# Kernel optimization log

Hardware: AMD Instinct MI355X
Metric: run time of the kernel (lower is better)

The kernel has to match this reference:

```python
import jax, jax.numpy as jnp
import numpy as np
import itertools

DIM_X, DIM_Y = 3, 3
MAX_DIGIT = DIM_X * DIM_Y          # 9
NUM_NODES = MAX_DIGIT ** 2         # 81
EMBED = 16
HID = 96
BATCH = 256
ITERS = 4


def determine_edges(dim_x, dim_y):
    md = dim_x * dim_y
    rows = []
    for r in range(md):
        for c in range(md):
            s = {(r, i) for i in range(md)} | {(i, c) for i in range(md)}
            xm, ym = r // dim_x * dim_x, c // dim_y * dim_y
            s |= set(itertools.product(range(xm, xm + dim_x), range(ym, ym + dim_y)))
            s -= {(r, c)}
            rows.append(sorted(i * md + j for i, j in s))
    return np.asarray(rows, dtype=np.int32)  # [81, 20]


def mlp3(x, w0, b0, w1, b1, w2, b2):
    # MLP([a,b,c,d]): two ReLU hidden layers, linear output
    x = jax.nn.relu(x @ w0.T + b0)
    x = jax.nn.relu(x @ w1.T + b1)
    return x @ w2.T + b2


def setup_inputs() -> dict:
    key = jax.random.key(0)
    keys = iter(jax.random.split(key, 40))

    def lin(din, dout):
        kw, kb = jax.random.split(next(keys))
        lim = 1.0 / np.sqrt(din)
        w = jax.random.uniform(kw, (dout, din), jnp.float32, -lim, lim)
        b = jax.random.uniform(kb, (dout,), jnp.float32, -lim, lim)
        return w, b

    embed = jax.random.normal(next(keys), (MAX_DIGIT + 1, EMBED), jnp.float32)

    in_w0, in_b0 = lin(EMBED, HID); in_w1, in_b1 = lin(HID, HID); in_w2, in_b2 = lin(HID, HID)
    f_w0, f_b0 = lin(2 * HID, HID); f_w1, f_b1 = lin(HID, HID); f_w2, f_b2 = lin(HID, HID)
    g_w0, g_b0 = lin(2 * HID, HID); g_w1, g_b1 = lin(HID, HID); g_w2, g_b2 = lin(HID, HID)
    r_w0, r_b0 = lin(HID, HID); r_w1, r_b1 = lin(HID, HID); r_w2, r_b2 = lin(HID, MAX_DIGIT)

    lim = 1.0 / np.sqrt(HID)
    lstm_wih = jax.random.uniform(next(keys), (4 * HID, HID), jnp.float32, -lim, lim)
    lstm_whh = jax.random.uniform(next(keys), (4 * HID, HID), jnp.float32, -lim, lim)
    lstm_bih = jax.random.uniform(next(keys), (4 * HID,), jnp.float32, -lim, lim)
    lstm_bhh = jax.random.uniform(next(keys), (4 * HID,), jnp.float32, -lim, lim)

    grids = jax.random.randint(next(keys), (BATCH, NUM_NODES), 0, MAX_DIGIT + 1)
    c0 = jax.random.normal(next(keys), (BATCH * NUM_NODES, HID), jnp.float32)
    edges = jnp.asarray(determine_edges(DIM_X, DIM_Y))

    return dict(embed=embed,
                in_w0=in_w0, in_b0=in_b0, in_w1=in_w1, in_b1=in_b1, in_w2=in_w2, in_b2=in_b2,
                f_w0=f_w0, f_b0=f_b0, f_w1=f_w1, f_b1=f_b1, f_w2=f_w2, f_b2=f_b2,
                g_w0=g_w0, g_b0=g_b0, g_w1=g_w1, g_b1=g_b1, g_w2=g_w2, g_b2=g_b2,
                lstm_wih=lstm_wih, lstm_whh=lstm_whh, lstm_bih=lstm_bih, lstm_bhh=lstm_bhh,
                r_w0=r_w0, r_b0=r_b0, r_w1=r_w1, r_b1=r_b1, r_w2=r_w2, r_b2=r_b2,
                c0=c0, grids=grids, edges=edges, iters=ITERS)


def reference(embed,
              in_w0, in_b0, in_w1, in_b1, in_w2, in_b2,
              f_w0, f_b0, f_w1, f_b1, f_w2, f_b2,
              g_w0, g_b0, g_w1, g_b1, g_w2, g_b2,
              lstm_wih, lstm_whh, lstm_bih, lstm_bhh,
              r_w0, r_b0, r_w1, r_b1, r_w2, r_b2,
              c0, grids, edges, iters):
    B, N = grids.shape
    K = edges.shape[1]
    emb = embed[grids]                                   # [B, N, EMBED]
    X = mlp3(emb, in_w0, in_b0, in_w1, in_b1, in_w2, in_b2)  # [B, N, HID]
    H = X
    h = X.reshape(B * N, HID)
    c = c0
    outputs = []
    for _ in range(iters):
        # gather neighbor states: [B, N, K, HID]
        Hn = H[:, edges]
        Hs = jnp.broadcast_to(H[:, :, None, :], Hn.shape)
        pair = jnp.concatenate([Hs, Hn], axis=-1)        # [B, N, K, 2*HID]
        M = mlp3(pair, f_w0, f_b0, f_w1, f_b1, f_w2, f_b2).sum(axis=2)  # [B, N, HID]
        gin = mlp3(jnp.concatenate([X, M], axis=-1),
                   g_w0, g_b0, g_w1, g_b1, g_w2, g_b2).reshape(B * N, HID)
        # single-step LSTM (torch gate order: i, f, g, o)
        gates = gin @ lstm_wih.T + lstm_bih + h @ lstm_whh.T + lstm_bhh
        gi, gf, gg, go = jnp.split(gates, 4, axis=-1)
        c = jax.nn.sigmoid(gf) * c + jax.nn.sigmoid(gi) * jnp.tanh(gg)
        h = jax.nn.sigmoid(go) * jnp.tanh(c)
        H = h.reshape(B, N, HID)
        outputs.append(mlp3(H, r_w0, r_b0, r_w1, r_b1, r_w2, r_b2))  # [B, N, MAX_DIGIT]
    return jnp.stack(outputs)  # [iters, B, N, MAX_DIGIT]
```

## Files before the change

### kernel.cpp

```cpp
#include <hip/hip_runtime.h>
#include <hip/hip_bf16.h>

typedef __hip_bfloat16 bf16;
typedef __attribute__((ext_vector_type(8))) short short8;
typedef __attribute__((ext_vector_type(8))) __bf16 bf16x8;
typedef __attribute__((ext_vector_type(4))) float f32x4;

#define BN 20736
#define NNODE 81
#define KNB 20

__device__ inline float bf2f(short s) {
  union { unsigned u; float f; } x; x.u = ((unsigned)(unsigned short)s) << 16; return x.f;
}
__device__ inline short f2bf(float f) {
  __hip_bfloat16 h = __float2bfloat16(f);
  return *reinterpret_cast<short*>(&h);
}
__device__ inline bf16x8 ld8(const bf16* p) {
  return __builtin_bit_cast(bf16x8, *(const short8*)p);
}

__device__ inline void zacc3(f32x4 acc[3]) {
  #pragma unroll
  for (int nt = 0; nt < 3; ++nt) acc[nt] = (f32x4){0.f, 0.f, 0.f, 0.f};
}
__device__ inline void load_w48(const bf16* __restrict__ W, int ldw, int n0, int lr, int lq,
                                bf16x8 wf[3][3]) {
  #pragma unroll
  for (int nt = 0; nt < 3; ++nt)
    #pragma unroll
    for (int ks = 0; ks < 3; ++ks)
      wf[nt][ks] = ld8(&W[(size_t)(n0 + nt * 16 + lr) * ldw + ks * 32 + lq * 8]);
}
__device__ inline void gemm48(const bf16x8 af[3], const bf16x8 wf[3][3], f32x4 acc[3]) {
  #pragma unroll
  for (int ks = 0; ks < 3; ++ks)
    #pragma unroll
    for (int nt = 0; nt < 3; ++nt)
      acc[nt] = __builtin_amdgcn_mfma_f32_16x16x32_bf16(af[ks], wf[nt][ks], acc[nt], 0, 0, 0);
}
__device__ inline void acc_store_cs(float* xw, const f32x4 acc[3], int lr, int lq, int n0) {
  #pragma unroll
  for (int nt = 0; nt < 3; ++nt)
    #pragma unroll
    for (int r = 0; r < 4; ++r)
      xw[(lq * 4 + r) * 100 + n0 + nt * 16 + lr] = acc[nt][r];
}
__device__ inline void xbuf_frag(const float* xw, int lr, int lq,
                                 const float* __restrict__ bias, float bscale,
                                 const bf16* residRow, int act,
                                 bf16x8 af[3]) {
  #pragma unroll
  for (int ks = 0; ks < 3; ++ks) {
    const int c0 = ks * 32 + lq * 8;
    float4 x0 = *(const float4*)&xw[lr * 100 + c0];
    float4 x1 = *(const float4*)&xw[lr * 100 + c0 + 4];
    float xv[8] = {x0.x, x0.y, x0.z, x0.w, x1.x, x1.y, x1.z, x1.w};
    if (bias) {
      float4 b0 = *(const float4*)&bias[c0];
      float4 b1 = *(const float4*)&bias[c0 + 4];
      float bv[8] = {b0.x, b0.y, b0.z, b0.w, b1.x, b1.y, b1.z, b1.w};
      #pragma unroll
      for (int j = 0; j < 8; ++j) xv[j] += bscale * bv[j];
    }
    if (residRow) {
      short8 r8 = *(const short8*)&residRow[c0];
      #pragma unroll
      for (int j = 0; j < 8; ++j) xv[j] += bf2f(r8[j]);
    }
    short8 o;
    #pragma unroll
    for (int j = 0; j < 8; ++j) {
      float v = xv[j];
      if (act) v = fmaxf(v, 0.f);
      o[j] = f2bf(v);
    }
    af[ks] = __builtin_bit_cast(bf16x8, o);
  }
}
__device__ inline void store_frag(bf16* dst, int lq, const bf16x8 af[3]) {
  #pragma unroll
  for (int ks = 0; ks < 3; ++ks)
    *(short8*)&dst[ks * 32 + lq * 8] = __builtin_bit_cast(short8, af[ks]);
}

__global__ __launch_bounds__(256) void prep_k(
    const float* in_w1, const float* in_w2, const float* f_w1, const float* f_w2,
    const float* g_w1, const float* g_w2, const float* r_w0, const float* r_w1,
    const float* r_w2, const float* wih, const float* whh, const float* g_w0,
    const float* f_w0, const float* in_w0, const float* f_b0,
    bf16* inw1b, bf16* inw2b, bf16* fw1b, bf16* fw2b,
    bf16* gw1b, bf16* gw2b, bf16* rw0b, bf16* rw1b,
    bf16* rw2b, bf16* wihb, bf16* whhb, bf16* gw0b,
    bf16* wfnb, bf16* w0pb, float* bias_fn)
{
  int idx = blockIdx.x * 256 + threadIdx.x;
  int y = blockIdx.y;
  const float* src = nullptr; bf16* dst = nullptr; int cnt = 0;
  switch (y) {
    case 0:  src = in_w1; dst = inw1b; cnt = 9216;  break;
    case 1:  src = in_w2; dst = inw2b; cnt = 9216;  break;
    case 2:  src = f_w1;  dst = fw1b;  cnt = 9216;  break;
    case 3:  src = f_w2;  dst = fw2b;  cnt = 9216;  break;
    case 4:  src = g_w1;  dst = gw1b;  cnt = 9216;  break;
    case 5:  src = g_w2;  dst = gw2b;  cnt = 9216;  break;
    case 6:  src = r_w0;  dst = rw0b;  cnt = 9216;  break;
    case 7:  src = r_w1;  dst = rw1b;  cnt = 9216;  break;
    case 8:  src = r_w2;  dst = rw2b;  cnt = 864;   break;
    case 9:  src = wih;   dst = wihb;  cnt = 36864; break;
    case 10: src = whh;   dst = whhb;  cnt = 36864; break;
    case 11: src = g_w0;  dst = gw0b;  cnt = 18432; break;
    case 12: {
      if (idx < 18432) {
        int n = idx / 96, k = idx - n * 96;
        float v = (n < 96) ? f_w0[n * 192 + k] : f_w0[(n - 96) * 192 + 96 + k];
        wfnb[idx] = __float2bfloat16(v);
      }
      return;
    }
    case 13: {
      if (idx < 3072) {
        int n = idx >> 5, k = idx & 31;
        w0pb[idx] = __float2bfloat16(k < 16 ? in_w0[n * 16 + k] : 0.f);
      }
      return;
    }
    default: {
      if (idx < 192) bias_fn[idx] = (idx < 96) ? f_b0[idx] : 0.f;
      return;
    }
  }
  if (idx < cnt) dst[idx] = __float2bfloat16(src[idx]);
}

__global__ __launch_bounds__(256) void prep2_k(
    const float* __restrict__ g_w0, const float* __restrict__ f_w2,
    const float* __restrict__ f_b2, const float* __restrict__ wih,
    const float* __restrict__ g_w2, const float* __restrict__ g_b2,
    const float* __restrict__ bih, const float* __restrict__ bhh,
    bf16* __restrict__ wmcb, float* __restrict__ b_mc,
    bf16* __restrict__ wgcb, float* __restrict__ b_lc)
{
  int idx = blockIdx.x * 256 + threadIdx.x;
  if (idx < 9216) {
    int n = idx / 96, k = idx - n * 96;
    float s = 0.f;
    for (int j = 0; j < 96; ++j) s += g_w0[n * 192 + 96 + j] * f_w2[j * 96 + k];
    wmcb[idx] = __float2bfloat16(s);
  } else if (idx < 9216 + 36864) {
    int r = idx - 9216;
    int m = r / 96, k = r - m * 96;
    float s = 0.f;
    for (int j = 0; j < 96; ++j) s += wih[m * 96 + j] * g_w2[j * 96 + k];
    wgcb[r] = __float2bfloat16(s);
  } else if (idx < 9216 + 36864 + 96) {
    int n = idx - 9216 - 36864;
    float s = 0.f;
    for (int j = 0; j < 96; ++j) s += g_w0[n * 192 + 96 + j] * 20.f * f_b2[j];
    b_mc[n] = s;
  } else if (idx < 9216 + 36864 + 96 + 384) {
    int m = idx - 9216 - 36864 - 96;
    float s = bih[m] + bhh[m];
    for (int j = 0; j < 96; ++j) s += wih[m * 96 + j] * g_b2[j];
    b_lc[m] = s;
  }
}

__global__ __launch_bounds__(256) void fused_in_k(
    const float* __restrict__ embed, const int* __restrict__ grids,
    const bf16* __restrict__ w0pb, const float* __restrict__ in_b0,
    const bf16* __restrict__ inw1b, const float* __restrict__ in_b1,
    const bf16* __restrict__ inw2b, const float* __restrict__ in_b2,
    const bf16* __restrict__ gw0b, const float* __restrict__ g_b0,
    const bf16* __restrict__ wfnb, const float* __restrict__ bias_fn,
    bf16* __restrict__ X, bf16* __restrict__ Xg, bf16* __restrict__ P)
{
  __shared__ float xbuf[2][2][1600];
  const int t = threadIdx.x, w = t >> 6, lane = t & 63, lr = lane & 15, lq = lane >> 4;
  const int mh = w >> 1, ch = w & 1, n0 = ch * 48;
  const int m0 = blockIdx.x * 32 + mh * 16;
  float* x0 = xbuf[0][mh];
  float* x1 = xbuf[1][mh];
  bf16x8 wf[3][3]; f32x4 acc[3]; bf16x8 af[3];

  short8 es = {0, 0, 0, 0, 0, 0, 0, 0};
  if (lq < 2) {
    int gidx = grids[m0 + lr];
    float4 e0 = *(const float4*)&embed[gidx * 16 + lq * 8];
    float4 e1 = *(const float4*)&embed[gidx * 16 + lq * 8 + 4];
    es[0] = f2bf(e0.x); es[1] = f2bf(e0.y); es[2] = f2bf(e0.z); es[3] = f2bf(e0.w);
    es[4] = f2bf(e1.x); es[5] = f2bf(e1.y); es[6] = f2bf(e1.z); es[7] = f2bf(e1.w);
  }
  bf16x8 a0 = __builtin_bit_cast(bf16x8, es);
  #pragma unroll
  for (int nt = 0; nt < 3; ++nt)
    wf[nt][0] = ld8(&w0pb[(size_t)(n0 + nt * 16 + lr) * 32 + lq * 8]);
  zacc3(acc);
  #pragma unroll
  for (int nt = 0; nt < 3; ++nt)
    acc[nt] = __builtin_amdgcn_mfma_f32_16x16x32_bf16(a0, wf[nt][0], acc[nt], 0, 0, 0);
  acc_store_cs(x0, acc, lr, lq, n0);
  __syncthreads();
  xbuf_frag(x0, lr, lq, in_b0, 1.f, nullptr, 1, af);
  load_w48(inw1b, 96, n0, lr, lq, wf); zacc3(acc); gemm48(af, wf, acc);
  acc_store_cs(x1, acc, lr, lq, n0);
  __syncthreads();
  xbuf_frag(x1, lr, lq, in_b1, 1.f, nullptr, 1, af);
  load_w48(inw2b, 96, n0, lr, lq, wf); zacc3(acc); gemm48(af, wf, acc);
  acc_store_cs(x0, acc, lr, lq, n0);
  __syncthreads();
  bf16x8 xf[3];
  xbuf_frag(x0, lr, lq, in_b2, 1.f, nullptr, 0, xf);
  if (ch == 0) store_frag(&X[(size_t)(m0 + lr) * 96], lq, xf);
  load_w48(gw0b, 192, n0, lr, lq, wf); zacc3(acc); gemm48(xf, wf, acc);
  acc_store_cs(x1, acc, lr, lq, n0);
  __syncthreads();
  xbuf_frag(x1, lr, lq, g_b0, 1.f, nullptr, 0, af);
  if (ch == 0) store_frag(&Xg[(size_t)(m0 + lr) * 96], lq, af);
  #pragma unroll
  for (int ph = 0; ph < 2; ++ph) {
    float* xb = ph ? x1 : x0;
    load_w48(wfnb + (size_t)ph * 96 * 96, 96, n0, lr, lq, wf); zacc3(acc); gemm48(xf, wf, acc);
    acc_store_cs(xb, acc, lr, lq, n0);
    __syncthreads();
    xbuf_frag(xb, lr, lq, bias_fn + ph * 96, 1.f, nullptr, 0, af);
    if (ch == 0) store_frag(&P[(size_t)(m0 + lr) * 192 + ph * 96], lq, af);
  }
}

__global__ __launch_bounds__(128) void edge_k(
    const bf16* __restrict__ P, const bf16* __restrict__ w1bf,
    const float* __restrict__ b1, const int* __restrict__ edges,
    bf16* __restrict__ S)
{
  __shared__ short zs[80 * 104];
  const int t = threadIdx.x;
  const int grp = (blockIdx.x & 7) * 648 + (blockIdx.x >> 3);
  const int w = t >> 6, lane = t & 63, lr = lane & 15, lq = lane >> 4;
  const int n0 = w * 48;

  bf16x8 wf1[3][3];
  #pragma unroll
  for (int nt = 0; nt < 3; ++nt)
    #pragma unroll
    for (int ks = 0; ks < 3; ++ks)
      wf1[nt][ks] = ld8(&w1bf[(size_t)(n0 + nt * 16 + lr) * 96 + ks * 32 + lq * 8]);
  float b1v[3];
  #pragma unroll
  for (int nt = 0; nt < 3; ++nt) b1v[nt] = b1[n0 + nt * 16 + lr];

  for (int cc = t; cc < 80 * 12; cc += 128) {
    int row = cc / 12, c8 = cc - row * 12;
    int p = row / 20, j = row - p * 20;
    int gr = grp * 4 + p;
    int b = gr / NNODE, i = gr - b * NNODE;
    int e = edges[i * KNB + j];
    short8 a8 = *(const short8*)&P[(size_t)gr * 192 + c8 * 8];
    short8 n8 = *(const short8*)&P[((size_t)b * NNODE + e) * 192 + 96 + c8 * 8];
    short8 z;
    #pragma unroll
    for (int q = 0; q < 8; ++q)
      z[q] = f2bf(fmaxf(bf2f(a8[q]) + bf2f(n8[q]), 0.f));
    *(short8*)&zs[row * 104 + c8 * 8] = z;
  }
  __syncthreads();

  f32x4 acc[5][3];
  #pragma unroll
  for (int mt = 0; mt < 5; ++mt)
    #pragma unroll
    for (int nt = 0; nt < 3; ++nt) acc[mt][nt] = (f32x4){0.f, 0.f, 0.f, 0.f};
  #pragma unroll
  for (int ks = 0; ks < 3; ++ks) {
    const int koff = ks * 32 + lq * 8;
    #pragma unroll
    for (int mt = 0; mt < 5; ++mt) {
      bf16x8 af = __builtin_bit_cast(bf16x8, *(const short8*)&zs[(mt * 16 + lr) * 104 + koff]);
      #pragma unroll
      for (int nt = 0; nt < 3; ++nt)
        acc[mt][nt] = __builtin_amdgcn_mfma_f32_16x16x32_bf16(af, wf1[nt][ks], acc[mt][nt], 0, 0, 0);
    }
  }

  float nodeacc[4][3];
  #pragma unroll
  for (int pp = 0; pp < 4; ++pp)
    #pragma unroll
    for (int nt = 0; nt < 3; ++nt) nodeacc[pp][nt] = 0.f;
  #pragma unroll
  for (int mt = 0; mt < 5; ++mt)
    #pragma unroll
    for (int nt = 0; nt < 3; ++nt)
      #pragma unroll
      for (int r = 0; r < 4; ++r) {
        int row = mt * 16 + lq * 4 + r;
        int p = row / 20;
        float v = fmaxf(acc[mt][nt][r] + b1v[nt], 0.f);
        #pragma unroll
        for (int pp = 0; pp < 4; ++pp)
          nodeacc[pp][nt] += (p == pp) ? v : 0.f;
      }
  #pragma unroll
  for (int pp = 0; pp < 4; ++pp)
    #pragma unroll
    for (int nt = 0; nt < 3; ++nt) {
      float v = nodeacc[pp][nt];
      v += __shfl_xor(v, 16, 64);
      v += __shfl_xor(v, 32, 64);
      if (lq == 0)
        S[(size_t)(grp * 4 + pp) * 96 + n0 + nt * 16 + lr] = __float2bfloat16(v);
    }
}

__global__ __launch_bounds__(128) void fused_iter_k(
    const bf16* __restrict__ Sin,
    const bf16* __restrict__ wmcb, const float* __restrict__ b_mc,
    const bf16* __restrict__ Xg,
    const bf16* __restrict__ gw1b, const float* __restrict__ g_b1,
    const bf16* __restrict__ Hin,
    const bf16* __restrict__ wgcb, const bf16* __restrict__ whhb,
    const float* __restrict__ b_lc,
    float* __restrict__ c, bf16* __restrict__ Hout,
    const bf16* __restrict__ wfnb, const float* __restrict__ bias_fn, bf16* __restrict__ P,
    const bf16* __restrict__ rw0b, const float* __restrict__ r_b0,
    const bf16* __restrict__ rw1b, const float* __restrict__ r_b1,
    const bf16* __restrict__ rw2b, const float* __restrict__ r_b2,
    float* __restrict__ outp, int doP)
{
  __shared__ float xb0[1600], xb1[1600];
  const int t = threadIdx.x, w = t >> 6, lane = t & 63, lr = lane & 15, lq = lane >> 4;
  const int n0 = w * 48;
  const int m0 = blockIdx.x * 16;

  bf16x8 wfA[3][3], wfB[3][3], af[3];
  f32x4 acc[3];

  #pragma unroll
  for (int ks = 0; ks < 3; ++ks)
    af[ks] = ld8(&Sin[(size_t)(m0 + lr) * 96 + ks * 32 + lq * 8]);
  bf16x8 hin[3];
  #pragma unroll
  for (int ks = 0; ks < 3; ++ks)
    hin[ks] = ld8(&Hin[(size_t)(m0 + lr) * 96 + ks * 32 + lq * 8]);

  load_w48(wmcb, 96, n0, lr, lq, wfA);
  zacc3(acc); gemm48(af, wfA, acc);
  load_w48(gw1b, 96, n0, lr, lq, wfB);
  acc_store_cs(xb0, acc, lr, lq, n0);
  __syncthreads();
  xbuf_frag(xb0, lr, lq, b_mc, 1.f, &Xg[(size_t)(m0 + lr) * 96], 1, af);
  zacc3(acc); gemm48(af, wfB, acc);
  acc_store_cs(xb1, acc, lr, lq, n0);
  float cv[3][4];
  #pragma unroll
  for (int nt = 0; nt < 3; ++nt)
    #pragma unroll
    for (int r = 0; r < 4; ++r)
      cv[nt][r] = c[(size_t)(m0 + lq * 4 + r) * 96 + n0 + nt * 16 + lr];
  __syncthreads();
  bf16x8 zf[3];
  xbuf_frag(xb1, lr, lq, g_b1, 1.f, nullptr, 1, zf);

  f32x4 ga[4][3];
  #pragma unroll
  for (int g4 = 0; g4 < 4; ++g4)
    #pragma unroll
    for (int nt = 0; nt < 3; ++nt) ga[g4][nt] = (f32x4){0.f, 0.f, 0.f, 0.f};
  #pragma unroll
  for (int g4 = 0; g4 < 4; ++g4)
    #pragma unroll
    for (int nt = 0; nt < 3; ++nt) {
      size_t nrow = (size_t)(g4 * 96 + n0 + nt * 16 + lr) * 96;
      #pragma unroll
      for (int ks = 0; ks < 3; ++ks) {
        ga[g4][nt] = __builtin_amdgcn_mfma_f32_16x16x32_bf16(
            zf[ks], ld8(&wgcb[nrow + ks * 32 + lq * 8]), ga[g4][nt], 0, 0, 0);
        ga[g4][nt] = __builtin_amdgcn_mfma_f32_16x16x32_bf16(
            hin[ks], ld8(&whhb[nrow + ks * 32 + lq * 8]), ga[g4][nt], 0, 0, 0);
      }
    }
  #pragma unroll
  for (int nt = 0; nt < 3; ++nt) {
    int col = n0 + nt * 16 + lr;
    float bvi = b_lc[col];
    float bvf = b_lc[96 + col];
    float bvg = b_lc[192 + col];
    float bvo = b_lc[288 + col];
    #pragma unroll
    for (int r = 0; r < 4; ++r) {
      int m = m0 + lq * 4 + r;
      size_t idx = (size_t)m * 96 + col;
      float gi = ga[0][nt][r] + bvi;
      float gfv = ga[1][nt][r] + bvf;
      float gg = ga[2][nt][r] + bvg;
      float go = ga[3][nt][r] + bvo;
      float si = 1.f / (1.f + expf(-gi));
      float sf = 1.f / (1.f + expf(-gfv));
      float so = 1.f / (1.f + expf(-go));
      float tg = tanhf(gg);
      float cn = sf * cv[nt][r] + si * tg;
      float ho = so * tanhf(cn);
      if (doP) {
        c[idx] = cn;
        Hout[idx] = __float2bfloat16(ho);
      }
      xb0[(lq * 4 + r) * 100 + col] = ho;
    }
  }
  __syncthreads();
  bf16x8 hf[3];
  xbuf_frag(xb0, lr, lq, nullptr, 0.f, nullptr, 0, hf);

  if (doP) {
    load_w48(wfnb, 96, n0, lr, lq, wfA);
    zacc3(acc); gemm48(hf, wfA, acc);
    load_w48(wfnb + 96 * 96, 96, n0, lr, lq, wfB);
    #pragma unroll
    for (int nt = 0; nt < 3; ++nt) {
      int col = n0 + nt * 16 + lr;
      float bvv = bias_fn[col];
      #pragma unroll
      for (int r = 0; r < 4; ++r)
        P[(size_t)(m0 + lq * 4 + r) * 192 + col] = __float2bfloat16(acc[nt][r] + bvv);
    }
    zacc3(acc); gemm48(hf, wfB, acc);
    #pragma unroll
    for (int nt = 0; nt < 3; ++nt) {
      int col = n0 + nt * 16 + lr;
      float bvv = bias_fn[96 + col];
      #pragma unroll
      for (int r = 0; r < 4; ++r)
        P[(size_t)(m0 + lq * 4 + r) * 192 + 96 + col] = __float2bfloat16(acc[nt][r] + bvv);
    }
  }

  load_w48(rw0b, 96, n0, lr, lq, wfA);
  zacc3(acc); gemm48(hf, wfA, acc);
  load_w48(rw1b, 96, n0, lr, lq, wfB);
  acc_store_cs(xb1, acc, lr, lq, n0);
  __syncthreads();
  xbuf_frag(xb1, lr, lq, r_b0, 1.f, nullptr, 1, af);
  zacc3(acc); gemm48(af, wfB, acc);
  acc_store_cs(xb0, acc, lr, lq, n0);
  __syncthreads();
  xbuf_frag(xb0, lr, lq, r_b1, 1.f, nullptr, 1, af);
  if (w == 0) {
    bf16x8 w9[3];
    #pragma unroll
    for (int ks = 0; ks < 3; ++ks) {
      short8 s = {0, 0, 0, 0, 0, 0, 0, 0};
      if (lr < 9) s = *(const short8*)&rw2b[(size_t)lr * 96 + ks * 32 + lq * 8];
      w9[ks] = __builtin_bit_cast(bf16x8, s);
    }
    f32x4 a9 = (f32x4){0.f, 0.f, 0.f, 0.f};
    #pragma unroll
    for (int ks = 0; ks < 3; ++ks)
      a9 = __builtin_amdgcn_mfma_f32_16x16x32_bf16(af[ks], w9[ks], a9, 0, 0, 0);
    if (lr < 9) {
      float bb = r_b2[lr];
      #pragma unroll
      for (int r = 0; r < 4; ++r)
        outp[(size_t)(m0 + lq * 4 + r) * 9 + lr] = a9[r] + bb;
    }
  }
}

extern "C" void kernel_launch(void* const* d_in, const int* in_sizes, int n_in,
                              void* d_out, int out_size, void* d_ws, size_t ws_size,
                              hipStream_t stream) {
  const float* embed   = (const float*)d_in[0];
  const float* in_w0   = (const float*)d_in[1];
  const float* in_b0   = (const float*)d_in[2];
  const float* in_w1   = (const float*)d_in[3];
  const float* in_b1   = (const float*)d_in[4];
  const float* in_w2   = (const float*)d_in[5];
  const float* in_b2   = (const float*)d_in[6];
  const float* f_w0    = (const float*)d_in[7];
  const float* f_b0    = (const float*)d_in[8];
  const float* f_w1    = (const float*)d_in[9];
  const float* f_b1    = (const float*)d_in[10];
  const float* f_w2    = (const float*)d_in[11];
  const float* f_b2    = (const float*)d_in[12];
  const float* g_w0    = (const float*)d_in[13];
  const float* g_b0    = (const float*)d_in[14];
  const float* g_w1    = (const float*)d_in[15];
  const float* g_b1    = (const float*)d_in[16];
  const float* g_w2    = (const float*)d_in[17];
  const float* g_b2    = (const float*)d_in[18];
  const float* wih     = (const float*)d_in[19];
  const float* whh     = (const float*)d_in[20];
  const float* bih     = (const float*)d_in[21];
  const float* bhh     = (const float*)d_in[22];
  const float* r_w0    = (const float*)d_in[23];
  const float* r_b0    = (const float*)d_in[24];
  const float* r_w1    = (const float*)d_in[25];
  const float* r_b1    = (const float*)d_in[26];
  const float* r_w2    = (const float*)d_in[27];
  const float* r_b2    = (const float*)d_in[28];
  const float* c0      = (const float*)d_in[29];
  const int*   grids   = (const int*)d_in[30];
  const int*   edges   = (const int*)d_in[31];

  float* out = (float*)d_out;
  const int iters = out_size / (BN * 9);

  float* c    = (float*)d_ws;
  bf16* H0    = (bf16*)(c + (size_t)BN * 96);
  bf16* H1    = H0 + (size_t)BN * 96;
  bf16* Xg    = H1 + (size_t)BN * 96;
  bf16* P     = Xg + (size_t)BN * 96;
  bf16* Sb    = P  + (size_t)BN * 192;
  bf16* w0pb  = Sb + (size_t)BN * 96;
  bf16* wfnb  = w0pb + 3072;
  bf16* inw1b = wfnb + 18432;
  bf16* inw2b = inw1b + 9216;
  bf16* fw1b  = inw2b + 9216;
  bf16* fw2b  = fw1b + 9216;
  bf16* gw0b  = fw2b + 9216;
  bf16* gw1b  = gw0b + 18432;
  bf16* gw2b  = gw1b + 9216;
  bf16* rw0b  = gw2b + 9216;
  bf16* rw1b  = rw0b + 9216;
  bf16* rw2b  = rw1b + 9216;
  bf16* wihb  = rw2b + 864;
  bf16* whhb  = wihb + 36864;
  bf16* wmcb  = whhb + 36864;
  bf16* wgcb  = wmcb + 9216;
  float* bias_fn = (float*)(wgcb + 36864);
  float* b_mc    = bias_fn + 192;
  float* b_lc    = b_mc + 96;

  prep_k<<<dim3(144, 15), 256, 0, stream>>>(
      in_w1, in_w2, f_w1, f_w2, g_w1, g_w2, r_w0, r_w1, r_w2, wih, whh, g_w0,
      f_w0, in_w0, f_b0,
      inw1b, inw2b, fw1b, fw2b, gw1b, gw2b, rw0b, rw1b, rw2b, wihb, whhb, gw0b,
      wfnb, w0pb, bias_fn);
  prep2_k<<<(9216 + 36864 + 480 + 255) / 256, 256, 0, stream>>>(
      g_w0, f_w2, f_b2, wih, g_w2, g_b2, bih, bhh, wmcb, b_mc, wgcb, b_lc);
  fused_in_k<<<BN / 32, 256, 0, stream>>>(embed, grids, w0pb, in_b0, inw1b, in_b1,
                                          inw2b, in_b2, gw0b, g_b0, wfnb, bias_fn,
                                          H0, Xg, P);
  hipMemcpyAsync(c, c0, (size_t)BN * 96 * sizeof(float), hipMemcpyDeviceToDevice, stream);

  for (int it = 0; it < iters; ++it) {
    bf16* Hin  = (it & 1) ? H1 : H0;
    bf16* Hout = (it & 1) ? H0 : H1;
    edge_k<<<BN / 4, 128, 0, stream>>>(P, fw1b, f_b1, edges, Sb);
    fused_iter_k<<<BN / 16, 128, 0, stream>>>(
        Sb, wmcb, b_mc, Xg, gw1b, g_b1,
        Hin, wgcb, whhb, b_lc, c, Hout,
        wfnb, bias_fn, P, rw0b, r_b0, rw1b, r_b1, rw2b, r_b2,
        out + (size_t)it * BN * 9, it < iters - 1 ? 1 : 0);
  }
}
```

Measured before the change: 315.3 us.

## Fuse all message-passing iterations into one cooperative persistent kernel

Replaces the per-iteration edge_k and fused_iter_k launches with a single cooperative kernel of 1296 blocks. Each block owns 16 nodes, keeps LSTM cell state, H and Xg fragments in registers across iterations, and uses grid.sync between iterations. P is double-buffered so neighbours can be read while the next projection is written. This removes kernel launch gaps and the global round trips for c, H and S. In exchange it depends on all blocks being co-resident, which requires 3 blocks per CU and higher register pressure, and falls back to the old path if the cooperative launch fails.

```diff
diff --git a/kernel.cpp b/kernel.cpp
--- a/kernel.cpp
+++ b/kernel.cpp
@@ -1,5 +1,8 @@
 #include <hip/hip_runtime.h>
 #include <hip/hip_bf16.h>
+#include <hip/hip_cooperative_groups.h>
+
+namespace cg = cooperative_groups;
 
 typedef __hip_bfloat16 bf16;
 typedef __attribute__((ext_vector_type(8))) short short8;
@@ -229,6 +232,258 @@
   }
 }
 
+__global__ __launch_bounds__(128, 3) void mega_iter_k(
+    bf16* __restrict__ P0, bf16* __restrict__ P1,
+    const bf16* __restrict__ w1bf, const float* __restrict__ b1,
+    const int* __restrict__ edges,
+    const bf16* __restrict__ wmcb, const float* __restrict__ b_mc,
+    const bf16* __restrict__ XgG,
+    const bf16* __restrict__ gw1b, const float* __restrict__ g_b1,
+    const bf16* __restrict__ H0in,
+    const bf16* __restrict__ wgcb, const bf16* __restrict__ whhb,
+    const float* __restrict__ b_lc, const float* __restrict__ c0,
+    const bf16* __restrict__ wfnb, const float* __restrict__ bias_fn,
+    const bf16* __restrict__ rw0b, const float* __restrict__ r_b0,
+    const bf16* __restrict__ rw1b, const float* __restrict__ r_b1,
+    const bf16* __restrict__ rw2b, const float* __restrict__ r_b2,
+    float* __restrict__ outp, int iters)
+{
+  __shared__ __align__(16) char ldsA[80 * 104 * 2];
+  __shared__ short sbuf[16 * 104];
+  short* zs  = (short*)ldsA;
+  float* xb0 = (float*)ldsA;
+  float* xb1 = (float*)(ldsA + 6400);
+  cg::grid_group grid = cg::this_grid();
+
+  const int t = threadIdx.x, w = t >> 6, lane = t & 63, lr = lane & 15, lq = lane >> 4;
+  const int n0 = w * 48;
+  const int blk = ((int)blockIdx.x & 7) * 162 + ((int)blockIdx.x >> 3);
+  const int m0 = blk * 16;
+
+  float cv[3][4];
+  #pragma unroll
+  for (int nt = 0; nt < 3; ++nt)
+    #pragma unroll
+    for (int r = 0; r < 4; ++r)
+      cv[nt][r] = c0[(size_t)(m0 + lq * 4 + r) * 96 + n0 + nt * 16 + lr];
+  bf16x8 hf[3];
+  #pragma unroll
+  for (int ks = 0; ks < 3; ++ks)
+    hf[ks] = ld8(&H0in[(size_t)(m0 + lr) * 96 + ks * 32 + lq * 8]);
+  bf16x8 xg[3];
+  #pragma unroll
+  for (int ks = 0; ks < 3; ++ks)
+    xg[ks] = ld8(&XgG[(size_t)(m0 + lr) * 96 + ks * 32 + lq * 8]);
+  bf16x8 wf1[3][3];
+  #pragma unroll
+  for (int nt = 0; nt < 3; ++nt)
+    #pragma unroll
+    for (int ks = 0; ks < 3; ++ks)
+      wf1[nt][ks] = ld8(&w1bf[(size_t)(n0 + nt * 16 + lr) * 96 + ks * 32 + lq * 8]);
+  float b1v[3];
+  #pragma unroll
+  for (int nt = 0; nt < 3; ++nt) b1v[nt] = b1[n0 + nt * 16 + lr];
+
+  for (int it = 0; it < iters; ++it) {
+    const bf16* Pc = (it & 1) ? P1 : P0;
+    bf16*       Pn = (it & 1) ? P0 : P1;
+
+    #pragma unroll 1
+    for (int rep = 0; rep < 4; ++rep) {
+      const int grp = (m0 >> 2) + rep;
+      for (int cc = t; cc < 80 * 12; cc += 128) {
+        int row = cc / 12, c8 = cc - row * 12;
+        int p = row / 20, j = row - p * 20;
+        int gr = grp * 4 + p;
+        int b = gr / NNODE, i = gr - b * NNODE;
+        int e = edges[i * KNB + j];
+        short8 a8 = *(const short8*)&Pc[(size_t)gr * 192 + c8 * 8];
+        short8 n8 = *(const short8*)&Pc[((size_t)b * NNODE + e) * 192 + 96 + c8 * 8];
+        short8 z;
+        #pragma unroll
+        for (int q = 0; q < 8; ++q)
+          z[q] = f2bf(fmaxf(bf2f(a8[q]) + bf2f(n8[q]), 0.f));
+        *(short8*)&zs[row * 104 + c8 * 8] = z;
+      }
+      __syncthreads();
+      f32x4 ea[5][3];
+      #pragma unroll
+      for (int mt = 0; mt < 5; ++mt)
+        #pragma unroll
+        for (int nt = 0; nt < 3; ++nt) ea[mt][nt] = (f32x4){0.f, 0.f, 0.f, 0.f};
+      #pragma unroll
+      for (int ks = 0; ks < 3; ++ks) {
+        const int koff = ks * 32 + lq * 8;
+        #pragma unroll
+        for (int mt = 0; mt < 5; ++mt) {
+          bf16x8 af = __builtin_bit_cast(bf16x8, *(const short8*)&zs[(mt * 16 + lr) * 104 + koff]);
+          #pragma unroll
+          for (int nt = 0; nt < 3; ++nt)
+            ea[mt][nt] = __builtin_amdgcn_mfma_f32_16x16x32_bf16(af, wf1[nt][ks], ea[mt][nt], 0, 0, 0);
+        }
+      }
+      float na[4][3];
+      #pragma unroll
+      for (int pp = 0; pp < 4; ++pp)
+        #pragma unroll
+        for (int nt = 0; nt < 3; ++nt) na[pp][nt] = 0.f;
+      #pragma unroll
+      for (int mt = 0; mt < 5; ++mt)
+        #pragma unroll
+        for (int nt = 0; nt < 3; ++nt)
+          #pragma unroll
+          for (int r = 0; r < 4; ++r) {
+            int row = mt * 16 + lq * 4 + r;
+            int p = row / 20;
+            float v = fmaxf(ea[mt][nt][r] + b1v[nt], 0.f);
+            #pragma unroll
+            for (int pp = 0; pp < 4; ++pp) na[pp][nt] += (p == pp) ? v : 0.f;
+          }
+      #pragma unroll
+      for (int pp = 0; pp < 4; ++pp)
+        #pragma unroll
+        for (int nt = 0; nt < 3; ++nt) {
+          float v = na[pp][nt];
+          v += __shfl_xor(v, 16, 64);
+          v += __shfl_xor(v, 32, 64);
+          if (lq == 0)
+            sbuf[(rep * 4 + pp) * 104 + n0 + nt * 16 + lr] = f2bf(v);
+        }
+      __syncthreads();
+    }
+
+    bf16x8 af[3], wfA[3][3], wfB[3][3];
+    f32x4 acc[3];
+    #pragma unroll
+    for (int ks = 0; ks < 3; ++ks)
+      af[ks] = ld8((const bf16*)&sbuf[lr * 104 + ks * 32 + lq * 8]);
+    load_w48(wmcb, 96, n0, lr, lq, wfA);
+    zacc3(acc); gemm48(af, wfA, acc);
+    load_w48(gw1b, 96, n0, lr, lq, wfB);
+    acc_store_cs(xb0, acc, lr, lq, n0);
+    __syncthreads();
+    #pragma unroll
+    for (int ks = 0; ks < 3; ++ks) {
+      const int c0_ = ks * 32 + lq * 8;
+      float4 x0_ = *(const float4*)&xb0[lr * 100 + c0_];
+      float4 x1_ = *(const float4*)&xb0[lr * 100 + c0_ + 4];
+      float xv[8] = {x0_.x, x0_.y, x0_.z, x0_.w, x1_.x, x1_.y, x1_.z, x1_.w};
+      float4 b0_ = *(const float4*)&b_mc[c0_];
+      float4 b1_ = *(const float4*)&b_mc[c0_ + 4];
+      float bv[8] = {b0_.x, b0_.y, b0_.z, b0_.w, b1_.x, b1_.y, b1_.z, b1_.w};
+      short8 xgs = __builtin_bit_cast(short8, xg[ks]);
+      short8 o;
+      #pragma unroll
+      for (int j = 0; j < 8; ++j)
+        o[j] = f2bf(fmaxf(xv[j] + bv[j] + bf2f(xgs[j]), 0.f));
+      af[ks] = __builtin_bit_cast(bf16x8, o);
+    }
+    zacc3(acc); gemm48(af, wfB, acc);
+    acc_store_cs(xb1, acc, lr, lq, n0);
+    __syncthreads();
+    bf16x8 zf[3];
+    xbuf_frag(xb1, lr, lq, g_b1, 1.f, nullptr, 1, zf);
+
+    f32x4 ga[4][3];
+    #pragma unroll
+    for (int g4 = 0; g4 < 4; ++g4)
+      #pragma unroll
+      for (int nt = 0; nt < 3; ++nt) ga[g4][nt] = (f32x4){0.f, 0.f, 0.f, 0.f};
+    #pragma unroll
+    for (int g4 = 0; g4 < 4; ++g4)
+      #pragma unroll
+      for (int nt = 0; nt < 3; ++nt) {
+        size_t nrow = (size_t)(g4 * 96 + n0 + nt * 16 + lr) * 96;
+        #pragma unroll
+        for (int ks = 0; ks < 3; ++ks) {
+          ga[g4][nt] = __builtin_amdgcn_mfma_f32_16x16x32_bf16(
+              zf[ks], ld8(&wgcb[nrow + ks * 32 + lq * 8]), ga[g4][nt], 0, 0, 0);
+          ga[g4][nt] = __builtin_amdgcn_mfma_f32_16x16x32_bf16(
+              hf[ks], ld8(&whhb[nrow + ks * 32 + lq * 8]), ga[g4][nt], 0, 0, 0);
+        }
+      }
+    #pragma unroll
+    for (int nt = 0; nt < 3; ++nt) {
+      int col = n0 + nt * 16 + lr;
+      float bvi = b_lc[col];
+      float bvf = b_lc[96 + col];
+      float bvg = b_lc[192 + col];
+      float bvo = b_lc[288 + col];
+      #pragma unroll
+      for (int r = 0; r < 4; ++r) {
+        float gi = ga[0][nt][r] + bvi;
+        float gfv = ga[1][nt][r] + bvf;
+        float gg = ga[2][nt][r] + bvg;
+        float go = ga[3][nt][r] + bvo;
+        float si = 1.f / (1.f + expf(-gi));
+        float sf = 1.f / (1.f + expf(-gfv));
+        float so = 1.f / (1.f + expf(-go));
+        float tg = tanhf(gg);
+        float cn = sf * cv[nt][r] + si * tg;
+        cv[nt][r] = cn;
+        xb0[(lq * 4 + r) * 100 + n0 + nt * 16 + lr] = so * tanhf(cn);
+      }
+    }
+    __syncthreads();
+    xbuf_frag(xb0, lr, lq, nullptr, 0.f, nullptr, 0, hf);
+
+    if (it < iters - 1) {
+      load_w48(wfnb, 96, n0, lr, lq, wfA);
+      zacc3(acc); gemm48(hf, wfA, acc);
+      load_w48(wfnb + 96 * 96, 96, n0, lr, lq, wfB);
+      #pragma unroll
+      for (int nt = 0; nt < 3; ++nt) {
+        int col = n0 + nt * 16 + lr;
+        float bvv = bias_fn[col];
+        #pragma unroll
+        for (int r = 0; r < 4; ++r)
+          Pn[(size_t)(m0 + lq * 4 + r) * 192 + col] = __float2bfloat16(acc[nt][r] + bvv);
+      }
+      zacc3(acc); gemm48(hf, wfB, acc);
+      #pragma unroll
+      for (int nt = 0; nt < 3; ++nt) {
+        int col = n0 + nt * 16 + lr;
+        float bvv = bias_fn[96 + col];
+        #pragma unroll
+        for (int r = 0; r < 4; ++r)
+          Pn[(size_t)(m0 + lq * 4 + r) * 192 + 96 + col] = __float2bfloat16(acc[nt][r] + bvv);
+      }
+    }
+
+    load_w48(rw0b, 96, n0, lr, lq, wfA);
+    zacc3(acc); gemm48(hf, wfA, acc);
+    load_w48(rw1b, 96, n0, lr, lq, wfB);
+    acc_store_cs(xb1, acc, lr, lq, n0);
+    __syncthreads();
+    xbuf_frag(xb1, lr, lq, r_b0, 1.f, nullptr, 1, af);
+    zacc3(acc); gemm48(af, wfB, acc);
+    acc_store_cs(xb0, acc, lr, lq, n0);
+    __syncthreads();
+    xbuf_frag(xb0, lr, lq, r_b1, 1.f, nullptr, 1, af);
+    if (w == 0) {
+      bf16x8 w9[3];
+      #pragma unroll
+      for (int ks = 0; ks < 3; ++ks) {
+        short8 s = {0, 0, 0, 0, 0, 0, 0, 0};
+        if (lr < 9) s = *(const short8*)&rw2b[(size_t)lr * 96 + ks * 32 + lq * 8];
+        w9[ks] = __builtin_bit_cast(bf16x8, s);
+      }
+      f32x4 a9 = (f32x4){0.f, 0.f, 0.f, 0.f};
+      #pragma unroll
+      for (int ks = 0; ks < 3; ++ks)
+        a9 = __builtin_amdgcn_mfma_f32_16x16x32_bf16(af[ks], w9[ks], a9, 0, 0, 0);
+      if (lr < 9) {
+        float bb = r_b2[lr];
+        #pragma unroll
+        for (int r = 0; r < 4; ++r)
+          outp[(size_t)it * BN * 9 + (size_t)(m0 + lq * 4 + r) * 9 + lr] = a9[r] + bb;
+      }
+    }
+
+    if (it < iters - 1) grid.sync();
+  }
+}
+
 __global__ __launch_bounds__(128) void edge_k(
     const bf16* __restrict__ P, const bf16* __restrict__ w1bf,
     const float* __restrict__ b1, const int* __restrict__ edges,
@@ -282,7 +537,6 @@
         acc[mt][nt] = __builtin_amdgcn_mfma_f32_16x16x32_bf16(af, wf1[nt][ks], acc[mt][nt], 0, 0, 0);
     }
   }
-
   float nodeacc[4][3];
   #pragma unroll
   for (int pp = 0; pp < 4; ++pp)
@@ -509,8 +763,9 @@
   bf16* H0    = (bf16*)(c + (size_t)BN * 96);
   bf16* H1    = H0 + (size_t)BN * 96;
   bf16* Xg    = H1 + (size_t)BN * 96;
-  bf16* P     = Xg + (size_t)BN * 96;
-  bf16* Sb    = P  + (size_t)BN * 192;
+  bf16* P0    = Xg + (size_t)BN * 96;
+  bf16* P1    = P0 + (size_t)BN * 192;
+  bf16* Sb    = P1 + (size_t)BN * 192;
   bf16* w0pb  = Sb + (size_t)BN * 96;
   bf16* wfnb  = w0pb + 3072;
   bf16* inw1b = wfnb + 18432;
@@ -540,17 +795,33 @@
       g_w0, f_w2, f_b2, wih, g_w2, g_b2, bih, bhh, wmcb, b_mc, wgcb, b_lc);
   fused_in_k<<<BN / 32, 256, 0, stream>>>(embed, grids, w0pb, in_b0, inw1b, in_b1,
                                           inw2b, in_b2, gw0b, g_b0, wfnb, bias_fn,
-                                          H0, Xg, P);
+                                          H0, Xg, P0);
   hipMemcpyAsync(c, c0, (size_t)BN * 96 * sizeof(float), hipMemcpyDeviceToDevice, stream);
+
+  {
+    int it_ = iters;
+    void* args[] = {
+      (void*)&P0, (void*)&P1, (void*)&fw1b, (void*)&f_b1, (void*)&edges,
+      (void*)&wmcb, (void*)&b_mc, (void*)&Xg, (void*)&gw1b, (void*)&g_b1,
+      (void*)&H0, (void*)&wgcb, (void*)&whhb, (void*)&b_lc, (void*)&c0,
+      (void*)&wfnb, (void*)&bias_fn, (void*)&rw0b, (void*)&r_b0,
+      (void*)&rw1b, (void*)&r_b1, (void*)&rw2b, (void*)&r_b2,
+      (void*)&out, (void*)&it_
+    };
+    hipError_t err = hipLaunchCooperativeKernel((const void*)mega_iter_k,
+                                                dim3(1296), dim3(128), args, 0, stream);
+    if (err == hipSuccess) return;
+    (void)hipGetLastError();
+  }
 
   for (int it = 0; it < iters; ++it) {
     bf16* Hin  = (it & 1) ? H1 : H0;
     bf16* Hout = (it & 1) ? H0 : H1;
-    edge_k<<<BN / 4, 128, 0, stream>>>(P, fw1b, f_b1, edges, Sb);
+    edge_k<<<BN / 4, 128, 0, stream>>>(P0, fw1b, f_b1, edges, Sb);
     fused_iter_k<<<BN / 16, 128, 0, stream>>>(
         Sb, wmcb, b_mc, Xg, gw1b, g_b1,
         Hin, wgcb, whhb, b_lc, c, Hout,
-        wfnb, bias_fn, P, rw0b, r_b0, rw1b, r_b1, rw2b, r_b2,
+        wfnb, bias_fn, P0, rw0b, r_b0, rw1b, r_b1, rw2b, r_b2,
         out + (size_t)it * BN * 9, it < iters - 1 ? 1 : 0);
   }
 }
```

Measured after the change: 1.205 ms. 3.82x slower.
